# Kernel tuning notes

Hardware: AMD Instinct MI355X
Metric: run time of the kernel (lower is better)

The kernel has to match this reference:

```python
import jax, jax.numpy as jnp
import numpy as np

N_BITS = 64
N_GROUPS = 8
P = N_BITS // N_GROUPS          # bits per group = 8
MAX_TABLE = 2 ** (P + N_GROUPS - 1)  # 32768, largest group-mapper table
BATCH = 524288


def setup_inputs() -> dict:
    key = jax.random.key(0)
    k1, k2, k3 = jax.random.split(key, 3)
    # input bit patterns [B, n_bits], values in {0,1}
    bits = jax.random.randint(k1, (BATCH, N_BITS), 0, 2, dtype=jnp.int32)
    # group mapper RAM tables, padded to max address space; table for group g
    # only uses the first 2^(P+g) addresses (addresses never exceed that range)
    group_tables = jax.random.uniform(k2, (N_GROUPS, P, MAX_TABLE), dtype=jnp.float32)
    # carry detector tables: one 1-neuron table per group boundary, binary outputs
    carry_tables = jax.random.randint(k3, (N_GROUPS - 1, 2 ** P), 0, 2, dtype=jnp.int32)
    return {"bits": bits, "group_tables": group_tables, "carry_tables": carry_tables}


def reference(bits, group_tables, carry_tables):
    B = bits.shape[0]
    gb = bits.reshape(B, N_GROUPS, P)                       # [B, G, P]
    # MSB-first address per group (matches reversed-bit enumeration in source)
    w = (2 ** (P - 1 - jnp.arange(P))).astype(jnp.int32)    # [P]
    gaddr = jnp.einsum('bgp,p->bg', gb, w)                  # [B, G] int32
    # carry detector g reads the raw bits of group g (independent of other carries)
    carries = carry_tables[jnp.arange(N_GROUPS - 1)[None, :],
                           gaddr[:, :N_GROUPS - 1]]          # [B, G-1] in {0,1}
    outs = []
    for g in range(N_GROUPS):  # small fixed loop over structurally distinct tables
        addr = gaddr[:, g]
        if g > 0:
            # mapper input = cat([group_bits, carries[0:g]]); group bits are high bits
            cw = (2 ** (g - 1 - jnp.arange(g))).astype(jnp.int32)
            addr = addr * (2 ** g) + carries[:, :g] @ cw
        # gather each neuron's table entry at this address -> [B, P]
        outs.append(jnp.take(group_tables[g], addr, axis=1).T)
    return jnp.stack(outs, axis=1).reshape(B, N_BITS)
```

## Files before the change

kernel.cpp:

```cpp
#include <hip/hip_runtime.h>

#define N_BITS    64
#define N_GROUPS  8
#define PDIM      8
#define MAX_TABLE 32768
#define BATCH     524288

typedef int   vi4 __attribute__((ext_vector_type(4)));
typedef float vf4 __attribute__((ext_vector_type(4)));

__global__ __launch_bounds__(256) void transpose_tables(
    const float* __restrict__ gt,
    float*       __restrict__ tt)
{
    const int i  = blockIdx.x * blockDim.x + threadIdx.x;
    const int a4 = i & (MAX_TABLE / 4 - 1);
    const int gp = i >> 13;
    const int p  = gp & 7;
    const int g  = gp >> 3;

    const vf4 v = reinterpret_cast<const vf4*>(gt)[i];
    const int a = a4 * 4;
    float* base = tt + (size_t)g * MAX_TABLE * PDIM + p;
    base[(size_t)(a + 0) * PDIM] = v.x;
    base[(size_t)(a + 1) * PDIM] = v.y;
    base[(size_t)(a + 2) * PDIM] = v.z;
    base[(size_t)(a + 3) * PDIM] = v.w;
}

__global__ __launch_bounds__(256) void comp_mapper_kernel(
    const int*   __restrict__ bits,
    const float* __restrict__ tab,
    const int*   __restrict__ ct,
    float*       __restrict__ out)
{
    const int tid = blockIdx.x * blockDim.x + threadIdx.x;
    const int g   = tid & 7;

    const vi4* bp = reinterpret_cast<const vi4*>(bits) + (size_t)tid * 2;
    vi4 x = __builtin_nontemporal_load(bp);
    vi4 y = __builtin_nontemporal_load(bp + 1);

    int gaddr = (x.x << 7) | (x.y << 6) | (x.z << 5) | (x.w << 4)
              | (y.x << 3) | (y.y << 2) | (y.z << 1) |  y.w;

    int carry = 0;
    if (g < 7) carry = ct[g * 256 + gaddr];

    unsigned long long m = __ballot(carry);
    const int lane = threadIdx.x & 63;
    const int base = lane & ~7;
    unsigned f = (unsigned)((m >> base) & 0xFFull);
    unsigned v = (__brev(f) >> 24) >> (8 - g);

    const int addr = (gaddr << g) | (int)v;

    const vf4* t = reinterpret_cast<const vf4*>(
        tab + ((size_t)g * MAX_TABLE + addr) * PDIM);
    vf4 o0 = t[0];
    vf4 o1 = t[1];

    vf4* op = reinterpret_cast<vf4*>(out) + (size_t)tid * 2;
    __builtin_nontemporal_store(o0, op);
    __builtin_nontemporal_store(o1, op + 1);
}

extern "C" void kernel_launch(void* const* d_in, const int* in_sizes, int n_in,
                              void* d_out, int out_size, void* d_ws, size_t ws_size,
                              hipStream_t stream) {
    const int*   bits = (const int*)  d_in[0];
    const float* gt   = (const float*)d_in[1];
    const int*   ct   = (const int*)  d_in[2];
    float*       out  = (float*)      d_out;

    const int total_threads = BATCH * N_GROUPS;
    const int block = 256;
    const int grid  = total_threads / block;

    float* tt = (float*)d_ws;
    const int t_threads = N_GROUPS * PDIM * MAX_TABLE / 4;
    transpose_tables<<<t_threads / block, block, 0, stream>>>(gt, tt);
    comp_mapper_kernel<<<grid, block, 0, stream>>>(bits, tt, ct, out);
}
```

Baseline: 282.2 us.

## Compact transposed tables and split gather across lane pairs handling two batch halves

The table transpose now writes only the used address range of each group, packed contiguously, and skips padding reads. This cuts transpose traffic and makes the workspace table smaller and more cache-friendly. The mapper kernel assigns two lanes per (row, group), each fetching one float4 half of the output. Each thread processes rows from both batch halves, so stores become fully contiguous float4 writes. In exchange, every thread loads its group's bits twice and does the carry ballot and bit compaction twice.

Result: faster. 266.4 us (-5.6%).

```diff
diff --git a/kernel.cpp b/kernel.cpp
--- a/kernel.cpp
+++ b/kernel.cpp
@@ -5,6 +5,7 @@
 #define PDIM      8
 #define MAX_TABLE 32768
 #define BATCH     524288
+#define HALF      (BATCH / 2)
 
 typedef int   vi4 __attribute__((ext_vector_type(4)));
 typedef float vf4 __attribute__((ext_vector_type(4)));
@@ -18,14 +19,16 @@
     const int gp = i >> 13;
     const int p  = gp & 7;
     const int g  = gp >> 3;
+    const int a  = a4 * 4;
+    if (a >= (256 << g)) return;
 
     const vf4 v = reinterpret_cast<const vf4*>(gt)[i];
-    const int a = a4 * 4;
-    float* base = tt + (size_t)g * MAX_TABLE * PDIM + p;
-    base[(size_t)(a + 0) * PDIM] = v.x;
-    base[(size_t)(a + 1) * PDIM] = v.y;
-    base[(size_t)(a + 2) * PDIM] = v.z;
-    base[(size_t)(a + 3) * PDIM] = v.w;
+    const int ro = 256 * ((1 << g) - 1);
+    float* base = tt + (size_t)(ro + a) * PDIM + p;
+    base[0 * PDIM] = v.x;
+    base[1 * PDIM] = v.y;
+    base[2 * PDIM] = v.z;
+    base[3 * PDIM] = v.w;
 }
 
 __global__ __launch_bounds__(256) void comp_mapper_kernel(
@@ -34,35 +37,59 @@
     const int*   __restrict__ ct,
     float*       __restrict__ out)
 {
-    const int tid = blockIdx.x * blockDim.x + threadIdx.x;
-    const int g   = tid & 7;
+    const int tid  = blockIdx.x * blockDim.x + threadIdx.x;
+    const int h    = tid & 1;
+    const int g    = (tid >> 1) & 7;
+    const int lane = threadIdx.x & 63;
 
-    const vi4* bp = reinterpret_cast<const vi4*>(bits) + (size_t)tid * 2;
-    vi4 x = __builtin_nontemporal_load(bp);
-    vi4 y = __builtin_nontemporal_load(bp + 1);
+    const size_t biA = (size_t)(tid >> 4) * 16 + (size_t)g * 2;
+    const vi4* bpA = reinterpret_cast<const vi4*>(bits) + biA;
+    const vi4* bpB = bpA + (size_t)HALF * 16;
+    vi4 xa = __builtin_nontemporal_load(bpA);
+    vi4 ya = __builtin_nontemporal_load(bpA + 1);
+    vi4 xb = __builtin_nontemporal_load(bpB);
+    vi4 yb = __builtin_nontemporal_load(bpB + 1);
 
-    int gaddr = (x.x << 7) | (x.y << 6) | (x.z << 5) | (x.w << 4)
-              | (y.x << 3) | (y.y << 2) | (y.z << 1) |  y.w;
+    int ga = (xa.x << 7) | (xa.y << 6) | (xa.z << 5) | (xa.w << 4)
+           | (ya.x << 3) | (ya.y << 2) | (ya.z << 1) |  ya.w;
+    int gb = (xb.x << 7) | (xb.y << 6) | (xb.z << 5) | (xb.w << 4)
+           | (yb.x << 3) | (yb.y << 2) | (yb.z << 1) |  yb.w;
 
-    int carry = 0;
-    if (g < 7) carry = ct[g * 256 + gaddr];
+    int cA = 0, cB = 0;
+    if (g < 7) {
+        cA = ct[g * 256 + ga];
+        cB = ct[g * 256 + gb];
+    }
 
-    unsigned long long m = __ballot(carry);
-    const int lane = threadIdx.x & 63;
-    const int base = lane & ~7;
-    unsigned f = (unsigned)((m >> base) & 0xFFull);
-    unsigned v = (__brev(f) >> 24) >> (8 - g);
+    unsigned long long mA = __ballot(cA);
+    unsigned long long mB = __ballot(cB);
+    const int base = lane & ~15;
+    unsigned fA = (unsigned)((mA >> base) & 0xFFFFull);
+    unsigned fB = (unsigned)((mB >> base) & 0xFFFFull);
 
-    const int addr = (gaddr << g) | (int)v;
+    unsigned eA = fA & 0x5555u;
+    eA = (eA | (eA >> 1)) & 0x3333u;
+    eA = (eA | (eA >> 2)) & 0x0F0Fu;
+    eA = (eA | (eA >> 4)) & 0x00FFu;
+    unsigned eB = fB & 0x5555u;
+    eB = (eB | (eB >> 1)) & 0x3333u;
+    eB = (eB | (eB >> 2)) & 0x0F0Fu;
+    eB = (eB | (eB >> 4)) & 0x00FFu;
 
-    const vf4* t = reinterpret_cast<const vf4*>(
-        tab + ((size_t)g * MAX_TABLE + addr) * PDIM);
-    vf4 o0 = t[0];
-    vf4 o1 = t[1];
+    unsigned vA = (__brev(eA) >> 24) >> (8 - g);
+    unsigned vB = (__brev(eB) >> 24) >> (8 - g);
 
-    vf4* op = reinterpret_cast<vf4*>(out) + (size_t)tid * 2;
-    __builtin_nontemporal_store(o0, op);
-    __builtin_nontemporal_store(o1, op + 1);
+    const int addrA = (ga << g) | (int)vA;
+    const int addrB = (gb << g) | (int)vB;
+
+    const int ro = 256 * ((1 << g) - 1);
+    const vf4* tt4 = reinterpret_cast<const vf4*>(tab);
+    vf4 oA = tt4[(size_t)(ro + addrA) * 2 + h];
+    vf4 oB = tt4[(size_t)(ro + addrB) * 2 + h];
+
+    vf4* op = reinterpret_cast<vf4*>(out);
+    __builtin_nontemporal_store(oA, op + tid);
+    __builtin_nontemporal_store(oB, op + tid + (size_t)HALF * 16);
 }
 
 extern "C" void kernel_launch(void* const* d_in, const int* in_sizes, int n_in,
@@ -73,12 +100,12 @@
     const int*   ct   = (const int*)  d_in[2];
     float*       out  = (float*)      d_out;
 
-    const int total_threads = BATCH * N_GROUPS;
     const int block = 256;
-    const int grid  = total_threads / block;
 
     float* tt = (float*)d_ws;
     const int t_threads = N_GROUPS * PDIM * MAX_TABLE / 4;
     transpose_tables<<<t_threads / block, block, 0, stream>>>(gt, tt);
-    comp_mapper_kernel<<<grid, block, 0, stream>>>(bits, tt, ct, out);
+
+    const int total_threads = BATCH * N_GROUPS;
+    comp_mapper_kernel<<<total_threads / block, block, 0, stream>>>(bits, tt, ct, out);
 }
```
